# Kernel tuning notes

Hardware: AMD Instinct MI355X
Metric: run time of the kernel (lower is better)

Reference implementation:

```python
import jax, jax.numpy as jnp
import numpy as np

# ---- static dims (match TextMMadapter / Hydra(d_model=128, d_state=16, d_conv=7, expand=2)) ----
HID = 4096          # LLM hidden size
DM = 128            # adapter bottleneck / hydra d_model
DIN = 2 * DM        # d_inner = expand * d_model = 256
DST = 16            # d_state
HD = 64             # headdim (Mamba2/Hydra default)
NH = DIN // HD      # nheads = 4
DCONV = 7
CONV_DIM = DIN + 2 * DST            # 288
DIN_PROJ = 2 * DIN + 2 * DST + 2 * NH  # 552
SEQ, BATCH = 2048, 4


def setup_inputs() -> dict:
    key = jax.random.key(0)
    ks = jax.random.split(key, 12)
    rn = lambda k, shape, s=0.02: jax.random.normal(k, shape, jnp.float32) * s
    dt = jnp.exp(jax.random.uniform(ks[5], (NH,), jnp.float32, np.log(1e-3), np.log(1e-1)))
    return dict(
        x=jax.random.normal(ks[0], (SEQ, BATCH, HID), jnp.float32),
        w_down=rn(ks[1], (DM, HID)), b_down=jnp.zeros((DM,), jnp.float32),
        w_up=rn(ks[2], (HID, DM)), b_up=jnp.zeros((HID,), jnp.float32),
        gate1=jnp.asarray(0.6, jnp.float32),
        hy_in_w=rn(ks[3], (DIN_PROJ, DM)),
        hy_conv_w=rn(ks[4], (CONV_DIM, 1, DCONV), 0.2),
        hy_conv_b=jnp.zeros((CONV_DIM,), jnp.float32),
        hy_dt_bias=jnp.log(jnp.expm1(dt)),               # inverse softplus of dt init
        hy_A_log=jnp.log(jax.random.uniform(ks[6], (NH,), jnp.float32, 1.0, 16.0)),
        hy_D=jnp.ones((NH,), jnp.float32),
        hy_fcD_w=rn(ks[7], (NH, DIN)),
        hy_norm_w=jnp.ones((DIN,), jnp.float32),
        hy_out_w=rn(ks[8], (DM, DIN)),
    )


def _causal_conv(x, w, b):
    # depthwise causal conv1d; x: (b,l,c), w: (c,1,k)
    y = jax.lax.conv_general_dilated(
        jnp.transpose(x, (0, 2, 1)), w, (1,), [(DCONV - 1, 0)],
        feature_group_count=CONV_DIM, dimension_numbers=("NCH", "OIH", "NCH"))
    return jnp.transpose(y, (0, 2, 1)) + b


def _ssm_scan(x, dt, A, B, C):
    # selective scan: h_t = exp(dt_t A) h_{t-1} + dt_t B_t x_t ; y_t = C_t . h_t
    # x:(b,l,h,p) dt:(b,l,h) A:(h,) B,C:(b,l,n)
    dA = jnp.exp(dt * A)            # (b,l,h)
    dBx = dt[..., None] * x         # (b,l,h,p)

    def step(h, t):
        dA_t, dBx_t, B_t, C_t = t
        h = dA_t[:, :, None, None] * h + dBx_t[..., None] * B_t[:, None, None, :]
        y = jnp.einsum("bhpn,bn->bhp", h, C_t)
        return h, y

    h0 = jnp.zeros((x.shape[0], NH, HD, DST), x.dtype)
    _, ys = jax.lax.scan(step, h0, (jnp.moveaxis(dA, 1, 0), jnp.moveaxis(dBx, 1, 0),
                                    jnp.moveaxis(B, 1, 0), jnp.moveaxis(C, 1, 0)))
    return jnp.moveaxis(ys, 0, 1)   # (b,l,h,p)


def _hydra(u, in_w, conv_w, conv_b, dt_bias, A_log, D, fcD_w, norm_w, out_w):
    b, l, _ = u.shape
    zxbcdt = u @ in_w.T                                   # (b,l,552)
    z = zxbcdt[..., :DIN]
    xBC = zxbcdt[..., DIN:DIN + CONV_DIM]
    dt2 = zxbcdt[..., DIN + CONV_DIM:]
    dt_fw = jax.nn.softplus(dt2[..., :NH] + dt_bias)
    dt_bw = jax.nn.softplus(jnp.flip(dt2[..., NH:], 1) + dt_bias)
    xBC = jax.nn.silu(_causal_conv(xBC, conv_w, conv_b))
    xs = xBC[..., :DIN]
    Bm = xBC[..., DIN:DIN + DST]
    Cm = xBC[..., DIN + DST:]
    A = -jnp.exp(A_log)
    x4 = xs.reshape(b, l, NH, HD)
    y_fw = _ssm_scan(x4, dt_fw, A, Bm, Cm).reshape(b, l, DIN)
    y_bw = jnp.flip(_ssm_scan(jnp.flip(x4, 1), dt_bw, A, jnp.flip(Bm, 1), jnp.flip(Cm, 1)).reshape(b, l, DIN), 1)
    zero = jnp.zeros((b, 1, DIN), u.dtype)
    # quasiseparable mixer: strictly-causal fw + strictly-anticausal bw + data-dependent diagonal
    y = jnp.concatenate([zero, y_fw[:, :-1]], 1) + jnp.concatenate([y_bw[:, 1:], zero], 1)
    y = y + xs * jnp.repeat(xs @ fcD_w.T + D, HD, axis=-1)
    yz = y * jax.nn.silu(z)                               # gated RMSNorm (norm after gate)
    y = yz * jax.lax.rsqrt(jnp.mean(jnp.square(yz), -1, keepdims=True) + 1e-5) * norm_w
    return y @ out_w.T


def reference(x, w_down, b_down, w_up, b_up, gate1, hy_in_w, hy_conv_w, hy_conv_b,
              hy_dt_bias, hy_A_log, hy_D, hy_fcD_w, hy_norm_w, hy_out_w):
    x_init = x                                            # (S,B,HID)
    h = x @ w_down.T + b_down                             # (S,B,128)
    h = jnp.transpose(h, (1, 0, 2))                       # (B,S,128)
    h = jax.nn.gelu(h, approximate=False)
    xmid = h
    hp = (hy_in_w, hy_conv_w, hy_conv_b, hy_dt_bias, hy_A_log, hy_D, hy_fcD_w, hy_norm_w, hy_out_w)
    h = _hydra(h, *hp)
    h = _hydra(h, *hp)
    alpha = jax.nn.sigmoid(gate1)
    h = alpha * xmid + (1.0 - alpha) * h
    h = xmid + h
    h = h @ w_up.T + b_up                                 # (B,S,HID)
    return x_init + jnp.transpose(h, (1, 0, 2))
```

## Files before the change

### kernel.cpp

```cpp
#include <hip/hip_runtime.h>
#include <hip/hip_bf16.h>
#include <math.h>

#define SEQL 2048
#define NB   4
#define HID  4096
#define DM   128
#define DIN  256
#define DST  16
#define HD   64
#define NH   4
#define CONV_DIM 288
#define DPROJ 552
#define MROWS (SEQL*NB)
#define TCH 64
#define NCHUNK (SEQL/TCH)

typedef __attribute__((ext_vector_type(8))) short short8;
typedef __attribute__((ext_vector_type(4))) float f32x4;

__device__ __forceinline__ float siluf(float v){ return v / (1.f + expf(-v)); }
__device__ __forceinline__ float geluf(float v){ return 0.5f*v*(1.f + erff(v*0.70710678118654752f)); }
__device__ __forceinline__ float wave_sum(float v){
    #pragma unroll
    for (int o = 32; o > 0; o >>= 1) v += __shfl_xor(v, o, 64);
    return v;
}
__device__ __forceinline__ unsigned bfpack2(float a, float b){
    __hip_bfloat162 v = __float22bfloat162_rn(make_float2(a, b));
    return *reinterpret_cast<unsigned*>(&v);
}

__global__ __launch_bounds__(256) void k_prep_w(const float* __restrict__ w_down,
    const float* __restrict__ w_up, const float* __restrict__ in_w,
    const float* __restrict__ out_w,
    __hip_bfloat16* __restrict__ wd, __hip_bfloat16* __restrict__ wu,
    __hip_bfloat16* __restrict__ wi, __hip_bfloat16* __restrict__ wo)
{
    int idx = blockIdx.x*256 + threadIdx.x;
    if (idx < 524288) { wd[idx] = __float2bfloat16(w_down[idx]); return; }
    idx -= 524288;
    if (idx < 524288) { wu[idx] = __float2bfloat16(w_up[idx]); return; }
    idx -= 524288;
    if (idx < 71680) { wi[idx] = (idx < 552*128) ? __float2bfloat16(in_w[idx]) : __float2bfloat16(0.f); return; }
    idx -= 71680;
    if (idx < 32768) { wo[idx] = __float2bfloat16(out_w[idx]); }
}

__global__ __launch_bounds__(256) void k_down_mfma(const float* __restrict__ x,
    const __hip_bfloat16* __restrict__ wbf, float* __restrict__ partial)
{
    __shared__ __align__(16) short Abuf[64][72];
    __shared__ __align__(16) short Wbuf[128][72];
    const int tid = threadIdx.x;
    const int m0 = blockIdx.x * 64;
    const int ks = blockIdx.y;
    const int b  = m0 >> 11, l0 = m0 & 2047;
    const int lane = tid & 63, wv = tid >> 6;
    const int fr = lane & 15, q = lane >> 4;
    f32x4 acc[8];
    #pragma unroll
    for (int i = 0; i < 8; ++i) acc[i] = (f32x4){0.f,0.f,0.f,0.f};

    const int arow = tid >> 2, aseg = tid & 3;
    const int wrow = tid >> 1, wseg = tid & 1;

    for (int k0 = ks*2048; k0 < ks*2048 + 2048; k0 += 64) {
        const float4* ap = (const float4*)(x + (size_t)((l0 + arow)*NB + b)*HID + k0 + aseg*16);
        float4 f0 = ap[0], f1 = ap[1], f2 = ap[2], f3 = ap[3];
        const uint4* wp = (const uint4*)(wbf + (size_t)wrow*HID + k0 + wseg*32);
        uint4 w0 = wp[0], w1 = wp[1], w2 = wp[2], w3 = wp[3];
        uint4 pk0, pk1;
        pk0.x = bfpack2(f0.x,f0.y); pk0.y = bfpack2(f0.z,f0.w);
        pk0.z = bfpack2(f1.x,f1.y); pk0.w = bfpack2(f1.z,f1.w);
        pk1.x = bfpack2(f2.x,f2.y); pk1.y = bfpack2(f2.z,f2.w);
        pk1.z = bfpack2(f3.x,f3.y); pk1.w = bfpack2(f3.z,f3.w);
        uint4* adst = (uint4*)&Abuf[arow][aseg*16];
        adst[0] = pk0; adst[1] = pk1;
        uint4* wdst = (uint4*)&Wbuf[wrow][wseg*32];
        wdst[0] = w0; wdst[1] = w1; wdst[2] = w2; wdst[3] = w3;
        __syncthreads();
        #pragma unroll
        for (int kh = 0; kh < 2; ++kh) {
            short8 af = *reinterpret_cast<const short8*>(&Abuf[wv*16 + fr][kh*32 + q*8]);
            #pragma unroll
            for (int ns = 0; ns < 8; ++ns) {
                short8 bf = *reinterpret_cast<const short8*>(&Wbuf[ns*16 + fr][kh*32 + q*8]);
                acc[ns] = __builtin_amdgcn_mfma_f32_16x16x32_bf16(af, bf, acc[ns], 0, 0, 0);
            }
        }
        __syncthreads();
    }
    #pragma unroll
    for (int ns = 0; ns < 8; ++ns)
        #pragma unroll
        for (int r = 0; r < 4; ++r)
            partial[((size_t)ks*MROWS + m0 + wv*16 + q*4 + r)*DM + ns*16 + fr] = acc[ns][r];
}

__global__ __launch_bounds__(256) void k_down_fix(const float* __restrict__ partial,
    const float* __restrict__ bias, float* __restrict__ xmid,
    __hip_bfloat16* __restrict__ ubf)
{
    size_t i4 = ((size_t)blockIdx.x*256 + threadIdx.x)*4;
    int n = (int)(i4 & (DM-1));
    float4 p0 = *(const float4*)&partial[i4];
    float4 p1 = *(const float4*)&partial[(size_t)MROWS*DM + i4];
    float4 bv = *(const float4*)&bias[n];
    float4 v;
    v.x = geluf(p0.x + p1.x + bv.x);
    v.y = geluf(p0.y + p1.y + bv.y);
    v.z = geluf(p0.z + p1.z + bv.z);
    v.w = geluf(p0.w + p1.w + bv.w);
    *(float4*)&xmid[i4] = v;
    uint2 pk; pk.x = bfpack2(v.x, v.y); pk.y = bfpack2(v.z, v.w);
    *(uint2*)&ubf[i4] = pk;
}

__global__ __launch_bounds__(256) void k_proj_in(const __hip_bfloat16* __restrict__ ubf,
    const __hip_bfloat16* __restrict__ wbf, float* __restrict__ zx)
{
    __shared__ __align__(16) short Abuf[64][136];
    __shared__ __align__(16) short Wbuf[80][136];
    const int tid = threadIdx.x;
    const int m0 = blockIdx.x*64;
    const int n0 = blockIdx.y*80;
    for (int i = tid; i < 64*16; i += 256) {
        int r = i >> 4, s = i & 15;
        *(uint4*)&Abuf[r][s*8] = *(const uint4*)&ubf[(size_t)(m0+r)*DM + s*8];
    }
    for (int i = tid; i < 80*16; i += 256) {
        int r = i >> 4, s = i & 15;
        *(uint4*)&Wbuf[r][s*8] = *(const uint4*)&wbf[(size_t)(n0+r)*DM + s*8];
    }
    __syncthreads();
    const int lane = tid & 63, wv = tid >> 6, fr = lane & 15, q = lane >> 4;
    f32x4 acc[5];
    #pragma unroll
    for (int i = 0; i < 5; ++i) acc[i] = (f32x4){0.f,0.f,0.f,0.f};
    #pragma unroll
    for (int kt = 0; kt < 4; ++kt) {
        short8 af = *reinterpret_cast<const short8*>(&Abuf[wv*16 + fr][kt*32 + q*8]);
        #pragma unroll
        for (int ns = 0; ns < 5; ++ns) {
            short8 bf = *reinterpret_cast<const short8*>(&Wbuf[ns*16 + fr][kt*32 + q*8]);
            acc[ns] = __builtin_amdgcn_mfma_f32_16x16x32_bf16(af, bf, acc[ns], 0, 0, 0);
        }
    }
    #pragma unroll
    for (int ns = 0; ns < 5; ++ns) {
        int n = n0 + ns*16 + fr;
        if (n < DPROJ) {
            #pragma unroll
            for (int r = 0; r < 4; ++r)
                zx[(size_t)(m0 + wv*16 + q*4 + r)*DPROJ + n] = acc[ns][r];
        }
    }
}

template<int PASS>
__global__ __launch_bounds__(256) void k_proj_out_t(const __hip_bfloat16* __restrict__ ynbf,
    const __hip_bfloat16* __restrict__ wbf, const float* __restrict__ xmid,
    const float* __restrict__ gate1,
    __hip_bfloat16* __restrict__ ubf, __hip_bfloat16* __restrict__ hcbf)
{
    __shared__ __align__(16) short Abuf[64][136];
    __shared__ __align__(16) short Wbuf[128][136];
    const int tid = threadIdx.x;
    const int m0 = blockIdx.x*64;
    const int lane = tid & 63, wv = tid >> 6, fr = lane & 15, q = lane >> 4;
    f32x4 acc[8];
    #pragma unroll
    for (int i = 0; i < 8; ++i) acc[i] = (f32x4){0.f,0.f,0.f,0.f};
    for (int kb = 0; kb < 2; ++kb) {
        if (kb) __syncthreads();
        for (int i = tid; i < 64*16; i += 256) {
            int r = i >> 4, s = i & 15;
            *(uint4*)&Abuf[r][s*8] = *(const uint4*)&ynbf[(size_t)(m0+r)*DIN + kb*128 + s*8];
        }
        for (int i = tid; i < 128*16; i += 256) {
            int r = i >> 4, s = i & 15;
            *(uint4*)&Wbuf[r][s*8] = *(const uint4*)&wbf[(size_t)r*DIN + kb*128 + s*8];
        }
        __syncthreads();
        #pragma unroll
        for (int kt = 0; kt < 4; ++kt) {
            short8 af = *reinterpret_cast<const short8*>(&Abuf[wv*16 + fr][kt*32 + q*8]);
            #pragma unroll
            for (int ns = 0; ns < 8; ++ns) {
                short8 bf = *reinterpret_cast<const short8*>(&Wbuf[ns*16 + fr][kt*32 + q*8]);
                acc[ns] = __builtin_amdgcn_mfma_f32_16x16x32_bf16(af, bf, acc[ns], 0, 0, 0);
            }
        }
    }
    float ca = 0.f, cb = 0.f;
    if (PASS == 1) {
        float al = 1.f / (1.f + expf(-gate1[0]));
        ca = 1.f + al; cb = 1.f - al;
    }
    #pragma unroll
    for (int ns = 0; ns < 8; ++ns)
        #pragma unroll
        for (int r = 0; r < 4; ++r) {
            int m = m0 + wv*16 + q*4 + r, n = ns*16 + fr;
            float v = acc[ns][r];
            if (PASS == 0) {
                ubf[(size_t)m*DM + n] = __float2bfloat16(v);
            } else {
                float xm = xmid[(size_t)m*DM + n];
                hcbf[(size_t)m*DM + n] = __float2bfloat16(ca*xm + cb*v);
            }
        }
}

__global__ __launch_bounds__(256) void k_up_mfma(const __hip_bfloat16* __restrict__ hc,
    const __hip_bfloat16* __restrict__ wbf, const float* __restrict__ b_up,
    const float* __restrict__ x, float* __restrict__ out)
{
    __shared__ __align__(16) short Abuf[64][136];
    __shared__ __align__(16) short Wbuf[128][136];
    const int tid = threadIdx.x;
    const int m0 = blockIdx.x*64;
    const int n0 = blockIdx.y*128;
    for (int i = tid; i < 64*16; i += 256) {
        int r = i >> 4, s = i & 15;
        *(uint4*)&Abuf[r][s*8] = *(const uint4*)&hc[(size_t)(m0+r)*DM + s*8];
    }
    for (int i = tid; i < 128*16; i += 256) {
        int r = i >> 4, s = i & 15;
        *(uint4*)&Wbuf[r][s*8] = *(const uint4*)&wbf[(size_t)(n0+r)*DM + s*8];
    }
    __syncthreads();
    const int lane = tid & 63, wv = tid >> 6, fr = lane & 15, q = lane >> 4;
    f32x4 acc[8];
    #pragma unroll
    for (int i = 0; i < 8; ++i) acc[i] = (f32x4){0.f,0.f,0.f,0.f};
    #pragma unroll
    for (int kt = 0; kt < 4; ++kt) {
        short8 af = *reinterpret_cast<const short8*>(&Abuf[wv*16 + fr][kt*32 + q*8]);
        #pragma unroll
        for (int ns = 0; ns < 8; ++ns) {
            short8 bf = *reinterpret_cast<const short8*>(&Wbuf[ns*16 + fr][kt*32 + q*8]);
            acc[ns] = __builtin_amdgcn_mfma_f32_16x16x32_bf16(af, bf, acc[ns], 0, 0, 0);
        }
    }
    #pragma unroll
    for (int r = 0; r < 4; ++r) {
        int m = m0 + wv*16 + q*4 + r;
        int b = m >> 11, l = m & 2047;
        size_t rowbase = (size_t)(l*NB + b)*HID + n0;
        #pragma unroll
        for (int ns = 0; ns < 8; ++ns) {
            int n = ns*16 + fr;
            out[rowbase + n] = acc[ns][r] + b_up[n0 + n] + x[rowbase + n];
        }
    }
}

__global__ __launch_bounds__(256) void k_conv(const float* __restrict__ zx,
    const float* __restrict__ cw, const float* __restrict__ cb,
    float* __restrict__ xBC)
{
    int idx = blockIdx.x*256 + threadIdx.x;
    if (idx >= MROWS*CONV_DIM) return;
    int c = idx % CONV_DIM;
    int m = idx / CONV_DIM;
    int l = m & 2047, b = m >> 11;
    float acc = cb[c];
    #pragma unroll
    for (int k = 0; k < 7; ++k) {
        int l2 = l - 6 + k;
        if (l2 >= 0)
            acc = fmaf(zx[(size_t)(b*SEQL + l2)*DPROJ + DIN + c], cw[c*7 + k], acc);
    }
    xBC[(size_t)m*CONV_DIM + c] = siluf(acc);
}

__global__ __launch_bounds__(64) void k_scan_state(const float* __restrict__ zx,
    const float* __restrict__ xBC, const float* __restrict__ dt_bias,
    const float* __restrict__ A_log, float* __restrict__ Sbuf, float* __restrict__ Pbuf)
{
    const int bid = blockIdx.x;
    const int c   = bid & (NCHUNK-1);
    const int h   = (bid >> 5) & (NH-1);
    const int b   = (bid >> 7) & 3;
    const int dir = bid >> 9;
    const int tid = threadIdx.x;
    __shared__ float dA_s[TCH], dt_s[TCH];
    __shared__ float Xs[TCH][HD];
    __shared__ float Bs[TCH][DST];
    {
        const int kk = tid;
        const int l = dir ? (SEQL-1 - (c*TCH + kk)) : (c*TCH + kk);
        float dtraw = zx[(size_t)(b*SEQL + l)*DPROJ + 544 + dir*NH + h] + dt_bias[h];
        float dt = dtraw > 20.f ? dtraw : log1pf(expf(dtraw));
        dt_s[kk] = dt;
        dA_s[kk] = expf(dt * (-expf(A_log[h])));
    }
    __syncthreads();
    #pragma unroll
    for (int t = 0; t < 16; ++t) {
        int k2 = t*4 + (tid >> 4);
        int p4 = (tid & 15)*4;
        int l2 = dir ? (SEQL-1 - (c*TCH + k2)) : (c*TCH + k2);
        float4 v = *(const float4*)&xBC[(size_t)(b*SEQL + l2)*CONV_DIM + h*HD + p4];
        float sc = dt_s[k2];
        v.x *= sc; v.y *= sc; v.z *= sc; v.w *= sc;
        *(float4*)&Xs[k2][p4] = v;
    }
    #pragma unroll
    for (int t = 0; t < 4; ++t) {
        int k2 = t*16 + (tid >> 2);
        int n4 = (tid & 3)*4;
        int l2 = dir ? (SEQL-1 - (c*TCH + k2)) : (c*TCH + k2);
        *(float4*)&Bs[k2][n4] = *(const float4*)&xBC[(size_t)(b*SEQL + l2)*CONV_DIM + DIN + n4];
    }
    __syncthreads();
    const int pg = tid >> 2, ng = tid & 3;
    float s[4][4];
    #pragma unroll
    for (int i = 0; i < 4; ++i)
        #pragma unroll
        for (int j = 0; j < 4; ++j) s[i][j] = 0.f;
    for (int k2 = 0; k2 < TCH; ++k2) {
        float dAv = dA_s[k2];
        float4 xv = *(const float4*)&Xs[k2][pg*4];
        float4 bv = *(const float4*)&Bs[k2][ng*4];
        float xa[4] = {xv.x, xv.y, xv.z, xv.w};
        float ba[4] = {bv.x, bv.y, bv.z, bv.w};
        #pragma unroll
        for (int i = 0; i < 4; ++i)
            #pragma unroll
            for (int j = 0; j < 4; ++j)
                s[i][j] = fmaf(dAv, s[i][j], xa[i]*ba[j]);
    }
    size_t sb = (size_t)bid * 1024;
    #pragma unroll
    for (int i = 0; i < 4; ++i) {
        float4 v = {s[i][0], s[i][1], s[i][2], s[i][3]};
        *(float4*)&Sbuf[sb + (size_t)((pg*4+i)*16 + ng*4)] = v;
    }
    {
        float pv = dA_s[tid];
        #pragma unroll
        for (int o = 32; o > 0; o >>= 1) pv *= __shfl_xor(pv, o, 64);
        if (tid == 0) Pbuf[bid] = pv;
    }
}

__global__ __launch_bounds__(64) void k_scan_combine2(const float* __restrict__ Sbuf,
    const float* __restrict__ Pbuf, float* __restrict__ Hbuf)
{
    const int gt = blockIdx.x*64 + threadIdx.x;
    const int g = gt >> 10, e = gt & 1023;
    float sv[NCHUNK], pw[NCHUNK];
    #pragma unroll
    for (int cc = 0; cc < NCHUNK; ++cc)
        sv[cc] = Sbuf[(size_t)(g*NCHUNK + cc)*1024 + e];
    #pragma unroll
    for (int cc = 0; cc < NCHUNK; ++cc)
        pw[cc] = Pbuf[g*NCHUNK + cc];
    float carry = 0.f;
    #pragma unroll
    for (int cc = 0; cc < NCHUNK; ++cc) {
        Hbuf[(size_t)(g*NCHUNK + cc)*1024 + e] = carry;
        carry = fmaf(pw[cc], carry, sv[cc]);
    }
}

__global__ __launch_bounds__(64) void k_scan_out(const float* __restrict__ zx,
    const float* __restrict__ xBC, const float* __restrict__ dt_bias,
    const float* __restrict__ A_log, const float* __restrict__ Hbuf,
    float* __restrict__ yfw, float* __restrict__ ybw)
{
    const int bid = blockIdx.x;
    const int c   = bid & (NCHUNK-1);
    const int h   = (bid >> 5) & (NH-1);
    const int b   = (bid >> 7) & 3;
    const int dir = bid >> 9;
    const int tid = threadIdx.x;
    __shared__ float dA_s[TCH], dt_s[TCH];
    __shared__ float Xs[TCH][HD];
    __shared__ float Bs[TCH][DST];
    __shared__ float Cs[TCH][DST];
    {
        const int kk = tid;
        const int l = dir ? (SEQL-1 - (c*TCH + kk)) : (c*TCH + kk);
        float dtraw = zx[(size_t)(b*SEQL + l)*DPROJ + 544 + dir*NH + h] + dt_bias[h];
        float dt = dtraw > 20.f ? dtraw : log1pf(expf(dtraw));
        dt_s[kk] = dt;
        dA_s[kk] = expf(dt * (-expf(A_log[h])));
    }
    __syncthreads();
    #pragma unroll
    for (int t = 0; t < 16; ++t) {
        int k2 = t*4 + (tid >> 4);
        int p4 = (tid & 15)*4;
        int l2 = dir ? (SEQL-1 - (c*TCH + k2)) : (c*TCH + k2);
        float4 v = *(const float4*)&xBC[(size_t)(b*SEQL + l2)*CONV_DIM + h*HD + p4];
        float sc = dt_s[k2];
        v.x *= sc; v.y *= sc; v.z *= sc; v.w *= sc;
        *(float4*)&Xs[k2][p4] = v;
    }
    #pragma unroll
    for (int t = 0; t < 4; ++t) {
        int k2 = t*16 + (tid >> 2);
        int n4 = (tid & 3)*4;
        int l2 = dir ? (SEQL-1 - (c*TCH + k2)) : (c*TCH + k2);
        *(float4*)&Bs[k2][n4] = *(const float4*)&xBC[(size_t)(b*SEQL + l2)*CONV_DIM + DIN + n4];
        *(float4*)&Cs[k2][n4] = *(const float4*)&xBC[(size_t)(b*SEQL + l2)*CONV_DIM + DIN + DST + n4];
    }
    __syncthreads();
    const int pg = tid >> 2, ng = tid & 3;
    float s[4][4];
    size_t hb = (size_t)bid * 1024;
    #pragma unroll
    for (int i = 0; i < 4; ++i) {
        float4 v = *(const float4*)&Hbuf[hb + (size_t)((pg*4+i)*16 + ng*4)];
        s[i][0] = v.x; s[i][1] = v.y; s[i][2] = v.z; s[i][3] = v.w;
    }
    float* yout = dir ? ybw : yfw;
    for (int k2 = 0; k2 < TCH; ++k2) {
        float dAv = dA_s[k2];
        float4 xv = *(const float4*)&Xs[k2][pg*4];
        float4 bv = *(const float4*)&Bs[k2][ng*4];
        float4 cv = *(const float4*)&Cs[k2][ng*4];
        float xa[4] = {xv.x, xv.y, xv.z, xv.w};
        float ba[4] = {bv.x, bv.y, bv.z, bv.w};
        float ca[4] = {cv.x, cv.y, cv.z, cv.w};
        float y[4];
        #pragma unroll
        for (int i = 0; i < 4; ++i) {
            #pragma unroll
            for (int j = 0; j < 4; ++j)
                s[i][j] = fmaf(dAv, s[i][j], xa[i]*ba[j]);
            y[i] = s[i][0]*ca[0] + s[i][1]*ca[1] + s[i][2]*ca[2] + s[i][3]*ca[3];
        }
        #pragma unroll
        for (int i = 0; i < 4; ++i) {
            y[i] += __shfl_xor(y[i], 1, 64);
            y[i] += __shfl_xor(y[i], 2, 64);
        }
        if (ng == 0) {
            int l2 = dir ? (SEQL-1 - (c*TCH + k2)) : (c*TCH + k2);
            float4 v = {y[0], y[1], y[2], y[3]};
            *(float4*)&yout[(size_t)(b*SEQL + l2)*DIN + h*HD + pg*4] = v;
        }
    }
}

__global__ __launch_bounds__(256) void k_epi(const float* __restrict__ zx,
    const float* __restrict__ xBC, const float* __restrict__ yfw,
    const float* __restrict__ ybw, const float* __restrict__ fcD_w,
    const float* __restrict__ Dv, const float* __restrict__ norm_w,
    __hip_bfloat16* __restrict__ ynbf)
{
    const int m = blockIdx.x;
    const int l = m & (SEQL-1);
    const int d = threadIdx.x;
    const int lane = d & 63, wave = d >> 6;
    __shared__ float red[4][4];
    __shared__ float redq[4];
    float xs = xBC[(size_t)m*CONV_DIM + d];
    float yv = 0.f;
    if (l > 0)       yv += yfw[(size_t)(m-1)*DIN + d];
    if (l < SEQL-1)  yv += ybw[(size_t)(m+1)*DIN + d];
    float p0 = wave_sum(xs * fcD_w[0*DIN + d]);
    float p1 = wave_sum(xs * fcD_w[1*DIN + d]);
    float p2 = wave_sum(xs * fcD_w[2*DIN + d]);
    float p3 = wave_sum(xs * fcD_w[3*DIN + d]);
    if (lane == 0) { red[wave][0]=p0; red[wave][1]=p1; red[wave][2]=p2; red[wave][3]=p3; }
    __syncthreads();
    const int h = d >> 6;
    float scal = red[0][h] + red[1][h] + red[2][h] + red[3][h] + Dv[h];
    yv = fmaf(xs, scal, yv);
    float z  = zx[(size_t)m*DPROJ + d];
    float yz = yv * siluf(z);
    float q = wave_sum(yz*yz);
    if (lane == 0) redq[wave] = q;
    __syncthreads();
    float ms = (redq[0] + redq[1] + redq[2] + redq[3]) * (1.f/DIN);
    float r = rsqrtf(ms + 1e-5f);
    ynbf[(size_t)m*DIN + d] = __float2bfloat16(yz * r * norm_w[d]);
}

extern "C" void kernel_launch(void* const* d_in, const int* in_sizes, int n_in,
                              void* d_out, int out_size, void* d_ws, size_t ws_size,
                              hipStream_t stream)
{
    const float* x       = (const float*)d_in[0];
    const float* w_down  = (const float*)d_in[1];
    const float* b_down  = (const float*)d_in[2];
    const float* w_up    = (const float*)d_in[3];
    const float* b_up    = (const float*)d_in[4];
    const float* gate1   = (const float*)d_in[5];
    const float* in_w    = (const float*)d_in[6];
    const float* conv_w  = (const float*)d_in[7];
    const float* conv_b  = (const float*)d_in[8];
    const float* dt_bias = (const float*)d_in[9];
    const float* A_log   = (const float*)d_in[10];
    const float* Dv      = (const float*)d_in[11];
    const float* fcD_w   = (const float*)d_in[12];
    const float* norm_w  = (const float*)d_in[13];
    const float* out_w   = (const float*)d_in[14];
    float* out = (float*)d_out;
    float* ws  = (float*)d_ws;

    size_t off = 0;
    float* xmid = ws + off; off += (size_t)MROWS*DM;
    float* zx   = ws + off; off += (size_t)MROWS*DPROJ;
    float* xBC  = ws + off; off += (size_t)MROWS*CONV_DIM;
    float* yfw  = ws + off; off += (size_t)MROWS*DIN;
    float* ybw  = ws + off; off += (size_t)MROWS*DIN;
    float* Sbuf = ws + off; off += (size_t)1024*1024;
    float* Pbuf = ws + off; off += 1024;
    float* Hbuf = ws + off; off += (size_t)1024*1024;
    __hip_bfloat16* bfb = (__hip_bfloat16*)(ws + off);
    size_t bo = 0;
    __hip_bfloat16* wd_bf = bfb + bo; bo += 524288;
    __hip_bfloat16* wu_bf = bfb + bo; bo += 524288;
    __hip_bfloat16* wi_bf = bfb + bo; bo += 71680;
    __hip_bfloat16* wo_bf = bfb + bo; bo += 32768;
    __hip_bfloat16* u_bf  = bfb + bo; bo += (size_t)MROWS*DM;
    __hip_bfloat16* yn_bf = bfb + bo; bo += (size_t)MROWS*DIN;
    __hip_bfloat16* hc_bf = bfb + bo; bo += (size_t)MROWS*DM;
    float* partial = zx;

    k_prep_w<<<4504, 256, 0, stream>>>(w_down, w_up, in_w, out_w, wd_bf, wu_bf, wi_bf, wo_bf);

    dim3 gdown(MROWS/64, 2);
    k_down_mfma<<<gdown, 256, 0, stream>>>(x, wd_bf, partial);
    k_down_fix<<<MROWS*DM/1024, 256, 0, stream>>>(partial, b_down, xmid, u_bf);

    for (int pass = 0; pass < 2; ++pass) {
        dim3 gin(MROWS/64, 7);
        k_proj_in<<<gin, 256, 0, stream>>>(u_bf, wi_bf, zx);
        k_conv<<<(MROWS*CONV_DIM)/256, 256, 0, stream>>>(zx, conv_w, conv_b, xBC);
        k_scan_state<<<1024, 64, 0, stream>>>(zx, xBC, dt_bias, A_log, Sbuf, Pbuf);
        k_scan_combine2<<<512, 64, 0, stream>>>(Sbuf, Pbuf, Hbuf);
        k_scan_out<<<1024, 64, 0, stream>>>(zx, xBC, dt_bias, A_log, Hbuf, yfw, ybw);
        k_epi<<<MROWS, 256, 0, stream>>>(zx, xBC, yfw, ybw, fcD_w, Dv, norm_w, yn_bf);
        if (pass == 0)
            k_proj_out_t<0><<<MROWS/64, 256, 0, stream>>>(yn_bf, wo_bf, xmid, gate1, u_bf, hc_bf);
        else
            k_proj_out_t<1><<<MROWS/64, 256, 0, stream>>>(yn_bf, wo_bf, xmid, gate1, u_bf, hc_bf);
    }

    dim3 gup(MROWS/64, HID/128);
    k_up_mfma<<<gup, 256, 0, stream>>>(hc_bf, wu_bf, b_up, x, out);
}
```

Measured before the change: 506.6 us.

## Widen scan blocks, precompute dt/dA in conv, raise down-proj K split

The scan state and output kernels now run 256 threads per block, with each thread owning one head-dim element and four state columns, where before 64 threads each owned a 4x4 register tile. This gives more parallelism and less per-thread serial work. The softplus/exp computation of dt and dA moves into the conv kernel, which writes chunk-ordered dt/dA buffers so the two scan kernels no longer recompute them. The down projection splits K four ways instead of two, adding more blocks at the cost of extra partial-sum traffic, which k_down_fix now reduces. The partial buffer aliases zx and must now hold 4x MROWS x DM floats.

```diff
diff --git a/kernel.cpp b/kernel.cpp
--- a/kernel.cpp
+++ b/kernel.cpp
@@ -15,6 +15,7 @@
 #define MROWS (SEQL*NB)
 #define TCH 64
 #define NCHUNK (SEQL/TCH)
+#define KSPLIT 4
 
 typedef __attribute__((ext_vector_type(8))) short short8;
 typedef __attribute__((ext_vector_type(4))) float f32x4;
@@ -65,7 +66,8 @@
     const int arow = tid >> 2, aseg = tid & 3;
     const int wrow = tid >> 1, wseg = tid & 1;
 
-    for (int k0 = ks*2048; k0 < ks*2048 + 2048; k0 += 64) {
+    const int kbase = ks * (HID/KSPLIT);
+    for (int k0 = kbase; k0 < kbase + HID/KSPLIT; k0 += 64) {
         const float4* ap = (const float4*)(x + (size_t)((l0 + arow)*NB + b)*HID + k0 + aseg*16);
         float4 f0 = ap[0], f1 = ap[1], f2 = ap[2], f3 = ap[3];
         const uint4* wp = (const uint4*)(wbf + (size_t)wrow*HID + k0 + wseg*32);
@@ -106,12 +108,14 @@
     int n = (int)(i4 & (DM-1));
     float4 p0 = *(const float4*)&partial[i4];
     float4 p1 = *(const float4*)&partial[(size_t)MROWS*DM + i4];
+    float4 p2 = *(const float4*)&partial[(size_t)2*MROWS*DM + i4];
+    float4 p3 = *(const float4*)&partial[(size_t)3*MROWS*DM + i4];
     float4 bv = *(const float4*)&bias[n];
     float4 v;
-    v.x = geluf(p0.x + p1.x + bv.x);
-    v.y = geluf(p0.y + p1.y + bv.y);
-    v.z = geluf(p0.z + p1.z + bv.z);
-    v.w = geluf(p0.w + p1.w + bv.w);
+    v.x = geluf(p0.x + p1.x + p2.x + p3.x + bv.x);
+    v.y = geluf(p0.y + p1.y + p2.y + p3.y + bv.y);
+    v.z = geluf(p0.z + p1.z + p2.z + p3.z + bv.z);
+    v.w = geluf(p0.w + p1.w + p2.w + p3.w + bv.w);
     *(float4*)&xmid[i4] = v;
     uint2 pk; pk.x = bfpack2(v.x, v.y); pk.y = bfpack2(v.z, v.w);
     *(uint2*)&ubf[i4] = pk;
@@ -257,28 +261,38 @@
     }
 }
 
-__global__ __launch_bounds__(256) void k_conv(const float* __restrict__ zx,
+__global__ __launch_bounds__(320) void k_conv(const float* __restrict__ zx,
     const float* __restrict__ cw, const float* __restrict__ cb,
-    float* __restrict__ xBC)
-{
-    int idx = blockIdx.x*256 + threadIdx.x;
-    if (idx >= MROWS*CONV_DIM) return;
-    int c = idx % CONV_DIM;
-    int m = idx / CONV_DIM;
-    int l = m & 2047, b = m >> 11;
-    float acc = cb[c];
-    #pragma unroll
-    for (int k = 0; k < 7; ++k) {
-        int l2 = l - 6 + k;
-        if (l2 >= 0)
-            acc = fmaf(zx[(size_t)(b*SEQL + l2)*DPROJ + DIN + c], cw[c*7 + k], acc);
-    }
-    xBC[(size_t)m*CONV_DIM + c] = siluf(acc);
-}
-
-__global__ __launch_bounds__(64) void k_scan_state(const float* __restrict__ zx,
-    const float* __restrict__ xBC, const float* __restrict__ dt_bias,
-    const float* __restrict__ A_log, float* __restrict__ Sbuf, float* __restrict__ Pbuf)
+    const float* __restrict__ dt_bias, const float* __restrict__ A_log,
+    float* __restrict__ xBC, float* __restrict__ dtbuf, float* __restrict__ dAbuf)
+{
+    const int m = blockIdx.x;
+    const int l = m & (SEQL-1), b = m >> 11;
+    const int c = threadIdx.x;
+    if (c < CONV_DIM) {
+        float acc = cb[c];
+        #pragma unroll
+        for (int k = 0; k < 7; ++k) {
+            int l2 = l - 6 + k;
+            if (l2 >= 0)
+                acc = fmaf(zx[(size_t)(b*SEQL + l2)*DPROJ + DIN + c], cw[c*7 + k], acc);
+        }
+        xBC[(size_t)m*CONV_DIM + c] = siluf(acc);
+    } else if (c < CONV_DIM + 2*NH) {
+        int j = c - CONV_DIM;
+        int dir = j >> 2, hh = j & 3;
+        float dtraw = zx[(size_t)(b*SEQL + l)*DPROJ + 544 + j] + dt_bias[hh];
+        float dt = dtraw > 20.f ? dtraw : log1pf(expf(dtraw));
+        float dA = expf(dt * (-expf(A_log[hh])));
+        int pos = dir ? (SEQL-1 - l) : l;
+        size_t o = (size_t)((dir*NH + hh)*NB + b)*SEQL + pos;
+        dtbuf[o] = dt; dAbuf[o] = dA;
+    }
+}
+
+__global__ __launch_bounds__(256) void k_scan_state(const float* __restrict__ xBC,
+    const float* __restrict__ dtbuf, const float* __restrict__ dAbuf,
+    float* __restrict__ Sbuf, float* __restrict__ Pbuf)
 {
     const int bid = blockIdx.x;
     const int c   = bid & (NCHUNK-1);
@@ -289,62 +303,48 @@
     __shared__ float dA_s[TCH], dt_s[TCH];
     __shared__ float Xs[TCH][HD];
     __shared__ float Bs[TCH][DST];
-    {
-        const int kk = tid;
-        const int l = dir ? (SEQL-1 - (c*TCH + kk)) : (c*TCH + kk);
-        float dtraw = zx[(size_t)(b*SEQL + l)*DPROJ + 544 + dir*NH + h] + dt_bias[h];
-        float dt = dtraw > 20.f ? dtraw : log1pf(expf(dtraw));
-        dt_s[kk] = dt;
-        dA_s[kk] = expf(dt * (-expf(A_log[h])));
-    }
-    __syncthreads();
-    #pragma unroll
-    for (int t = 0; t < 16; ++t) {
-        int k2 = t*4 + (tid >> 4);
-        int p4 = (tid & 15)*4;
+    const size_t tb = (size_t)((dir*NH + h)*NB + b)*SEQL + c*TCH;
+    if (tid < TCH) {
+        dt_s[tid] = dtbuf[tb + tid];
+        dA_s[tid] = dAbuf[tb + tid];
+    }
+    __syncthreads();
+    #pragma unroll
+    for (int t = 0; t < 4; ++t) {
+        int idx = t*256 + tid;
+        int k2 = idx >> 4, p4 = (idx & 15)*4;
         int l2 = dir ? (SEQL-1 - (c*TCH + k2)) : (c*TCH + k2);
         float4 v = *(const float4*)&xBC[(size_t)(b*SEQL + l2)*CONV_DIM + h*HD + p4];
         float sc = dt_s[k2];
         v.x *= sc; v.y *= sc; v.z *= sc; v.w *= sc;
         *(float4*)&Xs[k2][p4] = v;
     }
-    #pragma unroll
-    for (int t = 0; t < 4; ++t) {
-        int k2 = t*16 + (tid >> 2);
-        int n4 = (tid & 3)*4;
+    {
+        int k2 = tid >> 2, n4 = (tid & 3)*4;
         int l2 = dir ? (SEQL-1 - (c*TCH + k2)) : (c*TCH + k2);
         *(float4*)&Bs[k2][n4] = *(const float4*)&xBC[(size_t)(b*SEQL + l2)*CONV_DIM + DIN + n4];
     }
     __syncthreads();
-    const int pg = tid >> 2, ng = tid & 3;
-    float s[4][4];
-    #pragma unroll
-    for (int i = 0; i < 4; ++i)
-        #pragma unroll
-        for (int j = 0; j < 4; ++j) s[i][j] = 0.f;
+    const int lane = tid & 63, w = tid >> 6;
+    const int p = w*16 + (lane >> 2), ng = lane & 3;
+    float s[4] = {0.f, 0.f, 0.f, 0.f};
     for (int k2 = 0; k2 < TCH; ++k2) {
         float dAv = dA_s[k2];
-        float4 xv = *(const float4*)&Xs[k2][pg*4];
+        float xa  = Xs[k2][p];
         float4 bv = *(const float4*)&Bs[k2][ng*4];
-        float xa[4] = {xv.x, xv.y, xv.z, xv.w};
-        float ba[4] = {bv.x, bv.y, bv.z, bv.w};
-        #pragma unroll
-        for (int i = 0; i < 4; ++i)
-            #pragma unroll
-            for (int j = 0; j < 4; ++j)
-                s[i][j] = fmaf(dAv, s[i][j], xa[i]*ba[j]);
-    }
-    size_t sb = (size_t)bid * 1024;
-    #pragma unroll
-    for (int i = 0; i < 4; ++i) {
-        float4 v = {s[i][0], s[i][1], s[i][2], s[i][3]};
-        *(float4*)&Sbuf[sb + (size_t)((pg*4+i)*16 + ng*4)] = v;
-    }
-    {
-        float pv = dA_s[tid];
+        s[0] = fmaf(dAv, s[0], xa*bv.x);
+        s[1] = fmaf(dAv, s[1], xa*bv.y);
+        s[2] = fmaf(dAv, s[2], xa*bv.z);
+        s[3] = fmaf(dAv, s[3], xa*bv.w);
+    }
+    const size_t sb = (size_t)bid * 1024;
+    float4 sv = {s[0], s[1], s[2], s[3]};
+    *(float4*)&Sbuf[sb + (size_t)(p*16 + ng*4)] = sv;
+    if (w == 0) {
+        float pv = dA_s[lane];
         #pragma unroll
         for (int o = 32; o > 0; o >>= 1) pv *= __shfl_xor(pv, o, 64);
-        if (tid == 0) Pbuf[bid] = pv;
+        if (lane == 0) Pbuf[bid] = pv;
     }
 }
 
@@ -368,10 +368,9 @@
     }
 }
 
-__global__ __launch_bounds__(64) void k_scan_out(const float* __restrict__ zx,
-    const float* __restrict__ xBC, const float* __restrict__ dt_bias,
-    const float* __restrict__ A_log, const float* __restrict__ Hbuf,
-    float* __restrict__ yfw, float* __restrict__ ybw)
+__global__ __launch_bounds__(256) void k_scan_out(const float* __restrict__ xBC,
+    const float* __restrict__ dtbuf, const float* __restrict__ dAbuf,
+    const float* __restrict__ Hbuf, float* __restrict__ yfw, float* __restrict__ ybw)
 {
     const int bid = blockIdx.x;
     const int c   = bid & (NCHUNK-1);
@@ -383,68 +382,50 @@
     __shared__ float Xs[TCH][HD];
     __shared__ float Bs[TCH][DST];
     __shared__ float Cs[TCH][DST];
-    {
-        const int kk = tid;
-        const int l = dir ? (SEQL-1 - (c*TCH + kk)) : (c*TCH + kk);
-        float dtraw = zx[(size_t)(b*SEQL + l)*DPROJ + 544 + dir*NH + h] + dt_bias[h];
-        float dt = dtraw > 20.f ? dtraw : log1pf(expf(dtraw));
-        dt_s[kk] = dt;
-        dA_s[kk] = expf(dt * (-expf(A_log[h])));
-    }
-    __syncthreads();
-    #pragma unroll
-    for (int t = 0; t < 16; ++t) {
-        int k2 = t*4 + (tid >> 4);
-        int p4 = (tid & 15)*4;
+    const size_t tb = (size_t)((dir*NH + h)*NB + b)*SEQL + c*TCH;
+    if (tid < TCH) {
+        dt_s[tid] = dtbuf[tb + tid];
+        dA_s[tid] = dAbuf[tb + tid];
+    }
+    __syncthreads();
+    #pragma unroll
+    for (int t = 0; t < 4; ++t) {
+        int idx = t*256 + tid;
+        int k2 = idx >> 4, p4 = (idx & 15)*4;
         int l2 = dir ? (SEQL-1 - (c*TCH + k2)) : (c*TCH + k2);
         float4 v = *(const float4*)&xBC[(size_t)(b*SEQL + l2)*CONV_DIM + h*HD + p4];
         float sc = dt_s[k2];
         v.x *= sc; v.y *= sc; v.z *= sc; v.w *= sc;
         *(float4*)&Xs[k2][p4] = v;
     }
-    #pragma unroll
-    for (int t = 0; t < 4; ++t) {
-        int k2 = t*16 + (tid >> 2);
-        int n4 = (tid & 3)*4;
+    {
+        int k2 = tid >> 2, n4 = (tid & 3)*4;
         int l2 = dir ? (SEQL-1 - (c*TCH + k2)) : (c*TCH + k2);
         *(float4*)&Bs[k2][n4] = *(const float4*)&xBC[(size_t)(b*SEQL + l2)*CONV_DIM + DIN + n4];
         *(float4*)&Cs[k2][n4] = *(const float4*)&xBC[(size_t)(b*SEQL + l2)*CONV_DIM + DIN + DST + n4];
     }
     __syncthreads();
-    const int pg = tid >> 2, ng = tid & 3;
-    float s[4][4];
-    size_t hb = (size_t)bid * 1024;
-    #pragma unroll
-    for (int i = 0; i < 4; ++i) {
-        float4 v = *(const float4*)&Hbuf[hb + (size_t)((pg*4+i)*16 + ng*4)];
-        s[i][0] = v.x; s[i][1] = v.y; s[i][2] = v.z; s[i][3] = v.w;
-    }
+    const int lane = tid & 63, w = tid >> 6;
+    const int p = w*16 + (lane >> 2), ng = lane & 3;
+    const size_t hb = (size_t)bid * 1024;
+    float4 hv = *(const float4*)&Hbuf[hb + (size_t)(p*16 + ng*4)];
+    float s[4] = {hv.x, hv.y, hv.z, hv.w};
     float* yout = dir ? ybw : yfw;
     for (int k2 = 0; k2 < TCH; ++k2) {
         float dAv = dA_s[k2];
-        float4 xv = *(const float4*)&Xs[k2][pg*4];
+        float xa  = Xs[k2][p];
         float4 bv = *(const float4*)&Bs[k2][ng*4];
         float4 cv = *(const float4*)&Cs[k2][ng*4];
-        float xa[4] = {xv.x, xv.y, xv.z, xv.w};
-        float ba[4] = {bv.x, bv.y, bv.z, bv.w};
-        float ca[4] = {cv.x, cv.y, cv.z, cv.w};
-        float y[4];
-        #pragma unroll
-        for (int i = 0; i < 4; ++i) {
-            #pragma unroll
-            for (int j = 0; j < 4; ++j)
-                s[i][j] = fmaf(dAv, s[i][j], xa[i]*ba[j]);
-            y[i] = s[i][0]*ca[0] + s[i][1]*ca[1] + s[i][2]*ca[2] + s[i][3]*ca[3];
-        }
-        #pragma unroll
-        for (int i = 0; i < 4; ++i) {
-            y[i] += __shfl_xor(y[i], 1, 64);
-            y[i] += __shfl_xor(y[i], 2, 64);
-        }
+        s[0] = fmaf(dAv, s[0], xa*bv.x);
+        s[1] = fmaf(dAv, s[1], xa*bv.y);
+        s[2] = fmaf(dAv, s[2], xa*bv.z);
+        s[3] = fmaf(dAv, s[3], xa*bv.w);
+        float yp = s[0]*cv.x + s[1]*cv.y + s[2]*cv.z + s[3]*cv.w;
+        yp += __shfl_xor(yp, 1, 64);
+        yp += __shfl_xor(yp, 2, 64);
         if (ng == 0) {
             int l2 = dir ? (SEQL-1 - (c*TCH + k2)) : (c*TCH + k2);
-            float4 v = {y[0], y[1], y[2], y[3]};
-            *(float4*)&yout[(size_t)(b*SEQL + l2)*DIN + h*HD + pg*4] = v;
+            yout[(size_t)(b*SEQL + l2)*DIN + h*HD + p] = yp;
         }
     }
 }
@@ -515,6 +496,8 @@
     float* Sbuf = ws + off; off += (size_t)1024*1024;
     float* Pbuf = ws + off; off += 1024;
     float* Hbuf = ws + off; off += (size_t)1024*1024;
+    float* dtbuf= ws + off; off += (size_t)2*NH*NB*SEQL;
+    float* dAbuf= ws + off; off += (size_t)2*NH*NB*SEQL;
     __hip_bfloat16* bfb = (__hip_bfloat16*)(ws + off);
     size_t bo = 0;
     __hip_bfloat16* wd_bf = bfb + bo; bo += 524288;
@@ -528,17 +511,17 @@
 
     k_prep_w<<<4504, 256, 0, stream>>>(w_down, w_up, in_w, out_w, wd_bf, wu_bf, wi_bf, wo_bf);
 
-    dim3 gdown(MROWS/64, 2);
+    dim3 gdown(MROWS/64, KSPLIT);
     k_down_mfma<<<gdown, 256, 0, stream>>>(x, wd_bf, partial);
     k_down_fix<<<MROWS*DM/1024, 256, 0, stream>>>(partial, b_down, xmid, u_bf);
 
     for (int pass = 0; pass < 2; ++pass) {
         dim3 gin(MROWS/64, 7);
         k_proj_in<<<gin, 256, 0, stream>>>(u_bf, wi_bf, zx);
-        k_conv<<<(MROWS*CONV_DIM)/256, 256, 0, stream>>>(zx, conv_w, conv_b, xBC);
-        k_scan_state<<<1024, 64, 0, stream>>>(zx, xBC, dt_bias, A_log, Sbuf, Pbuf);
+        k_conv<<<MROWS, 320, 0, stream>>>(zx, conv_w, conv_b, dt_bias, A_log, xBC, dtbuf, dAbuf);
+        k_scan_state<<<1024, 256, 0, stream>>>(xBC, dtbuf, dAbuf, Sbuf, Pbuf);
         k_scan_combine2<<<512, 64, 0, stream>>>(Sbuf, Pbuf, Hbuf);
-        k_scan_out<<<1024, 64, 0, stream>>>(zx, xBC, dt_bias, A_log, Hbuf, yfw, ybw);
+        k_scan_out<<<1024, 256, 0, stream>>>(xBC, dtbuf, dAbuf, Hbuf, yfw, ybw);
         k_epi<<<MROWS, 256, 0, stream>>>(zx, xBC, yfw, ybw, fcD_w, Dv, norm_w, yn_bf);
         if (pass == 0)
             k_proj_out_t<0><<<MROWS/64, 256, 0, stream>>>(yn_bf, wo_bf, xmid, gate1, u_bf, hc_bf);
```

Result: no change. 503.9 us (-0.5%).
